# Kernel optimization log

Measured on AMD Instinct MI355X. Metric: run time of the kernel, lower is better.

Reference implementation:

```python
import jax, jax.numpy as jnp
import numpy as np

H, KVH, D, BS, L = 32, 8, 128, 16, 4096
MAX_BLOCKS = L // BS          # 256 blocks per sequence (sink cache capacity)
B = 16
NUM_BLOCKS = B * MAX_BLOCKS   # 4096 total cache blocks
T = MAX_BLOCKS * BS           # 4096 linearized cache slots per sequence
SCALE = 1.0 / np.sqrt(D)


def _rope_cos_sin(pos):
    # neox-style RoPE tables; pos: int array [...]. returns cos/sin [..., D/2]
    inv_freq = 1.0 / (10000.0 ** (jnp.arange(0, D, 2, dtype=jnp.float32) / D))
    ang = pos[..., None].astype(jnp.float32) * inv_freq
    return jnp.cos(ang), jnp.sin(ang)


def _apply_rope(x, cos, sin):
    # x [..., D]; cos/sin broadcastable to x[..., :D//2]
    x1, x2 = jnp.split(x, 2, axis=-1)
    return jnp.concatenate([x1 * cos - x2 * sin, x2 * cos + x1 * sin], axis=-1)


def setup_inputs() -> dict:
    key = jax.random.key(0)
    ks = jax.random.split(key, 6)
    q = jax.random.normal(ks[0], (B, H * D), dtype=jnp.float32)
    k = jax.random.normal(ks[1], (B, KVH * D), dtype=jnp.float32)
    v = jax.random.normal(ks[2], (B, KVH * D), dtype=jnp.float32)
    key_cache = jax.random.normal(ks[3], (NUM_BLOCKS, BS, KVH, D), dtype=jnp.float32)
    value_cache = jax.random.normal(ks[4], (NUM_BLOCKS, BS, KVH, D), dtype=jnp.float32)
    block_tables = jnp.arange(B * MAX_BLOCKS, dtype=jnp.int32).reshape(B, MAX_BLOCKS)
    context_lens = jax.random.randint(ks[5], (B,), 0, 6000, dtype=jnp.int32)
    return {"q": q, "k": k, "v": v, "key_cache": key_cache,
            "value_cache": value_cache, "block_tables": block_tables,
            "context_lens": context_lens}


def reference(q, k, v, key_cache, value_cache, block_tables, context_lens):
    ctx = context_lens.astype(jnp.int32)                         # [B] past tokens
    rem = ctx % BS
    # sink/rolling cap: if past >= model_context_len, effective seq len caps
    seq_len = jnp.where(ctx >= L, L - BS + rem + 1, ctx + 1)     # [B]
    pos_q = seq_len - 1                                          # capped current position

    # gather pre-rope keys/values from paged cache -> [B, T, KVH, D]
    keys = key_cache[block_tables].reshape(B, T, KVH, D)
    vals = value_cache[block_tables].reshape(B, T, KVH, D)

    # re-apply rope to gathered keys at their cache-relative positions 0..T-1
    cos_k, sin_k = _rope_cos_sin(jnp.arange(T))                  # [T, D/2]
    keys = _apply_rope(keys, cos_k[None, :, None, :], sin_k[None, :, None, :])

    # rope current q, k at capped positions
    cos_q, sin_q = _rope_cos_sin(pos_q)                          # [B, D/2]
    qh = _apply_rope(q.reshape(B, H, D), cos_q[:, None, :], sin_q[:, None, :])
    kh = _apply_rope(k.reshape(B, KVH, D), cos_q[:, None, :], sin_q[:, None, :])

    # scatter current token's k/v at its slot (offset rem in last used block == seq_len-1)
    bidx = jnp.arange(B)
    keys = keys.at[bidx, pos_q].set(kh)
    vals = vals.at[bidx, pos_q].set(v.reshape(B, KVH, D))

    # GQA attention over first seq_len cached tokens
    G = H // KVH
    qg = qh.reshape(B, KVH, G, D)
    scores = jnp.einsum('bhgd,bthd->bhgt', qg, keys) * SCALE     # [B, KVH, G, T]
    mask = jnp.arange(T)[None, :] < seq_len[:, None]             # [B, T]
    scores = jnp.where(mask[:, None, None, :], scores, jnp.finfo(scores.dtype).min)
    probs = jax.nn.softmax(scores, axis=-1)
    out = jnp.einsum('bhgt,bthd->bhgd', probs, vals)             # [B, KVH, G, D]
    return out.reshape(B, H * D)
```

## Files before the change

### kernel.cpp

```cpp
#include <hip/hip_runtime.h>
#include <math.h>

#define B_      16
#define H_      32
#define KVH_    8
#define G_      4
#define D_      128
#define BS_     16
#define L_      4096
#define MAXB_   256
#define T_      4096
#define NPART_  16
#define PART_   256
#define SCALE_  0.08838834764831843f

__device__ __forceinline__ int seq_len_of(int ctx) {
  return (ctx >= L_) ? (L_ - BS_ + (ctx & (BS_ - 1)) + 1) : (ctx + 1);
}


#define LOADK(P, tt)                                                        \
  {                                                                         \
    int blk_  = sblk[((tt) - t0) >> 4];                                     \
    int base_ = ((blk_ * BS_ + ((tt) & (BS_ - 1))) * KVH_ + kvh) * D_;      \
    const float4* kc4_ = (const float4*)(kc + base_);                       \
    const float4* vc4_ = (const float4*)(vc + base_);                       \
    P##ka = kc4_[dg];      P##kb = kc4_[16 + dg];                           \
    P##va = vc4_[dg];      P##vb = vc4_[16 + dg];                           \
  }

#define COMPUTE(P, tt)                                                      \
  {                                                                         \
    float kr1[4], kr2[4];                                                   \
    kr1[0] = P##ka.x * cc0.x - P##kb.x * cc0.y;                             \
    kr2[0] = P##kb.x * cc0.x + P##ka.x * cc0.y;                             \
    kr1[1] = P##ka.y * cc0.z - P##kb.y * cc0.w;                             \
    kr2[1] = P##kb.y * cc0.z + P##ka.y * cc0.w;                             \
    kr1[2] = P##ka.z * cc1.x - P##kb.z * cc1.y;                             \
    kr2[2] = P##kb.z * cc1.x + P##ka.z * cc1.y;                             \
    kr1[3] = P##ka.w * cc1.z - P##kb.w * cc1.w;                             \
    kr2[3] = P##kb.w * cc1.z + P##ka.w * cc1.w;                             \
    bool valid_ = ((tt) != posq);                                           \
    float s[G_];                                                            \
    _Pragma("unroll")                                                       \
    for (int g = 0; g < G_; ++g) {                                          \
      s[g] = kr1[0] * q1[g][0] + kr2[0] * q2[g][0]                          \
           + kr1[1] * q1[g][1] + kr2[1] * q2[g][1]                          \
           + kr1[2] * q1[g][2] + kr2[2] * q2[g][2]                          \
           + kr1[3] * q1[g][3] + kr2[3] * q2[g][3];                         \
    }                                                                       \
    _Pragma("unroll")                                                       \
    for (int off = 1; off <= 8; off <<= 1) {                                \
      _Pragma("unroll")                                                     \
      for (int g = 0; g < G_; ++g) s[g] += __shfl_xor(s[g], off);           \
    }                                                                       \
    _Pragma("unroll")                                                       \
    for (int g = 0; g < G_; ++g) {                                          \
      float sv   = valid_ ? s[g] : -1e30f;                                  \
      float mn   = fmaxf(m[g], sv);                                         \
      float corr = __expf(m[g] - mn);                                       \
      float p    = __expf(sv - mn);                                         \
      p = valid_ ? p : 0.0f;                                                \
      m[g] = mn;                                                            \
      l[g] = l[g] * corr + p;                                               \
      acc[g][0] = acc[g][0] * corr + p * P##va.x;                           \
      acc[g][1] = acc[g][1] * corr + p * P##va.y;                           \
      acc[g][2] = acc[g][2] * corr + p * P##va.z;                           \
      acc[g][3] = acc[g][3] * corr + p * P##va.w;                           \
      acc[g][4] = acc[g][4] * corr + p * P##vb.x;                           \
      acc[g][5] = acc[g][5] * corr + p * P##vb.y;                           \
      acc[g][6] = acc[g][6] * corr + p * P##vb.z;                           \
      acc[g][7] = acc[g][7] * corr + p * P##vb.w;                           \
    }                                                                       \
    {                     \
      float nc_;                                                            \
      nc_ = cc0.x * r0.x - cc0.y * r0.y;                                    \
      cc0.y = cc0.y * r0.x + cc0.x * r0.y; cc0.x = nc_;                     \
      nc_ = cc0.z * r0.z - cc0.w * r0.w;                                    \
      cc0.w = cc0.w * r0.z + cc0.z * r0.w; cc0.z = nc_;                     \
      nc_ = cc1.x * r1.x - cc1.y * r1.y;                                    \
      cc1.y = cc1.y * r1.x + cc1.x * r1.y; cc1.x = nc_;                     \
      nc_ = cc1.z * r1.z - cc1.w * r1.w;                                    \
      cc1.w = cc1.w * r1.z + cc1.z * r1.w; cc1.z = nc_;                     \
    }                                                                       \
  }

__global__ __launch_bounds__(256) void attn_partial_kernel(
    const float* __restrict__ q, const float* __restrict__ knew,
    const float* __restrict__ vnew, const float* __restrict__ kc,
    const float* __restrict__ vc, const int* __restrict__ btab,
    const int* __restrict__ ctxl,
    float* __restrict__ opart, float2* __restrict__ ml) {
  int bid  = blockIdx.x;
  int part = bid & (NPART_ - 1);
  int kvh  = (bid >> 4) & (KVH_ - 1);
  int b    = bid >> 7;

  int seq = seq_len_of(ctxl[b]);
  int t0 = part * PART_;
  if (t0 >= seq) return;
  int t1 = min(t0 + PART_, seq);
  int posq = seq - 1;

  int lane = threadIdx.x & 63;
  int wave = threadIdx.x >> 6;
  int tsub = lane >> 4;
  int dg   = lane & 15;

  __shared__ int sblk[PART_ / BS_];
  if (threadIdx.x < PART_ / BS_)
    sblk[threadIdx.x] = btab[b * MAXB_ + (t0 >> 4) + threadIdx.x];
  __syncthreads();

  int tstart = t0 + 4 * wave + tsub;
  float4 cc0, cc1, r0, r1, cq0, cq1;
  {
    float ft = (float)tstart, fq = (float)posq;
    float cs[3][8];
#pragma unroll
    for (int j = 0; j < 4; ++j) {
      double invd = pow(10000.0, -(double)(8 * dg + 2 * j) / 128.0);
      float invf = (float)invd;
      float angs[3] = {ft * invf, 16.0f * invf, fq * invf};
#pragma unroll
      for (int u = 0; u < 3; ++u) {
        double sn, csn;
        sincos((double)angs[u], &sn, &csn);
        cs[u][2 * j]     = (float)csn;
        cs[u][2 * j + 1] = (float)sn;
      }
    }
    cc0 = make_float4(cs[0][0], cs[0][1], cs[0][2], cs[0][3]);
    cc1 = make_float4(cs[0][4], cs[0][5], cs[0][6], cs[0][7]);
    r0  = make_float4(cs[1][0], cs[1][1], cs[1][2], cs[1][3]);
    r1  = make_float4(cs[1][4], cs[1][5], cs[1][6], cs[1][7]);
    cq0 = make_float4(cs[2][0], cs[2][1], cs[2][2], cs[2][3]);
    cq1 = make_float4(cs[2][4], cs[2][5], cs[2][6], cs[2][7]);
  }

  float q1[G_][4], q2[G_][4];
#pragma unroll
  for (int g = 0; g < G_; ++g) {
    const float* qp = q + b * (H_ * D_) + (kvh * G_ + g) * D_;
    float4 a  = *(const float4*)(qp + 4 * dg);
    float4 bq = *(const float4*)(qp + 64 + 4 * dg);
    q1[g][0] = (a.x * cq0.x - bq.x * cq0.y) * SCALE_;
    q2[g][0] = (bq.x * cq0.x + a.x * cq0.y) * SCALE_;
    q1[g][1] = (a.y * cq0.z - bq.y * cq0.w) * SCALE_;
    q2[g][1] = (bq.y * cq0.z + a.y * cq0.w) * SCALE_;
    q1[g][2] = (a.z * cq1.x - bq.z * cq1.y) * SCALE_;
    q2[g][2] = (bq.z * cq1.x + a.z * cq1.y) * SCALE_;
    q1[g][3] = (a.w * cq1.z - bq.w * cq1.w) * SCALE_;
    q2[g][3] = (bq.w * cq1.z + a.w * cq1.w) * SCALE_;
  }

  float m[G_], l[G_], acc[G_][8];
#pragma unroll
  for (int g = 0; g < G_; ++g) {
    m[g] = -1e30f; l[g] = 0.f;
#pragma unroll
    for (int j = 0; j < 8; ++j) acc[g][j] = 0.f;
  }

  {
    float4 Aka, Akb, Ava, Avb;
    float4 Bka, Bkb, Bva, Bvb;
    int t = tstart;
    if (t < t1) {
      LOADK(A, t);
      while (1) {
        int t2 = t + 16;
        if (t2 < t1) LOADK(B, t2);
        COMPUTE(A, t);
        t = t2;
        if (t >= t1) break;
        t2 = t + 16;
        if (t2 < t1) LOADK(A, t2);
        COMPUTE(B, t);
        t = t2;
        if (t >= t1) break;
      }
    }
  }

  if (threadIdx.x < 16 && posq >= t0 && posq < t1) {
    const float* kp = knew + (b * KVH_ + kvh) * D_;
    float4 xa = *(const float4*)(kp + 4 * dg);
    float4 xb = *(const float4*)(kp + 64 + 4 * dg);
    float kr1[4], kr2[4];
    kr1[0] = xa.x * cq0.x - xb.x * cq0.y;  kr2[0] = xb.x * cq0.x + xa.x * cq0.y;
    kr1[1] = xa.y * cq0.z - xb.y * cq0.w;  kr2[1] = xb.y * cq0.z + xa.y * cq0.w;
    kr1[2] = xa.z * cq1.x - xb.z * cq1.y;  kr2[2] = xb.z * cq1.x + xa.z * cq1.y;
    kr1[3] = xa.w * cq1.z - xb.w * cq1.w;  kr2[3] = xb.w * cq1.z + xa.w * cq1.w;
    const float* vp = vnew + (b * KVH_ + kvh) * D_;
    float4 va_ = *(const float4*)(vp + 4 * dg);
    float4 vb_ = *(const float4*)(vp + 64 + 4 * dg);
    float s[G_];
#pragma unroll
    for (int g = 0; g < G_; ++g) {
      s[g] = kr1[0] * q1[g][0] + kr2[0] * q2[g][0]
           + kr1[1] * q1[g][1] + kr2[1] * q2[g][1]
           + kr1[2] * q1[g][2] + kr2[2] * q2[g][2]
           + kr1[3] * q1[g][3] + kr2[3] * q2[g][3];
    }
#pragma unroll
    for (int off = 1; off <= 8; off <<= 1) {
#pragma unroll
      for (int g = 0; g < G_; ++g) s[g] += __shfl_xor(s[g], off);
    }
#pragma unroll
    for (int g = 0; g < G_; ++g) {
      float sv   = s[g];
      float mn   = fmaxf(m[g], sv);
      float corr = __expf(m[g] - mn);
      float p    = __expf(sv - mn);
      m[g] = mn;
      l[g] = l[g] * corr + p;
      acc[g][0] = acc[g][0] * corr + p * va_.x;
      acc[g][1] = acc[g][1] * corr + p * va_.y;
      acc[g][2] = acc[g][2] * corr + p * va_.z;
      acc[g][3] = acc[g][3] * corr + p * va_.w;
      acc[g][4] = acc[g][4] * corr + p * vb_.x;
      acc[g][5] = acc[g][5] * corr + p * vb_.y;
      acc[g][6] = acc[g][6] * corr + p * vb_.z;
      acc[g][7] = acc[g][7] * corr + p * vb_.w;
    }
  }

  auto merge_off = [&](int off) {
#pragma unroll
    for (int g = 0; g < G_; ++g) {
      float mo = __shfl_xor(m[g], off);
      float lo = __shfl_xor(l[g], off);
      float M  = fmaxf(m[g], mo);
      float fa = __expf(m[g] - M);
      float fb = __expf(mo - M);
      l[g] = l[g] * fa + lo * fb;
      m[g] = M;
#pragma unroll
      for (int j = 0; j < 8; ++j) {
        float ao = __shfl_xor(acc[g][j], off);
        acc[g][j] = acc[g][j] * fa + ao * fb;
      }
    }
  };
  merge_off(16);
  merge_off(32);

  __shared__ float  lds_acc[4][G_][D_];
  __shared__ float2 lds_ml[4][G_];
  if (lane < 16) {
#pragma unroll
    for (int g = 0; g < G_; ++g) {
#pragma unroll
      for (int j = 0; j < 8; ++j) {
        int dim = (j < 4) ? (4 * dg + j) : (64 + 4 * dg + (j - 4));
        lds_acc[wave][g][dim] = acc[g][j];
      }
      if (lane == 0) lds_ml[wave][g] = make_float2(m[g], l[g]);
    }
  }
  __syncthreads();
  if (wave == 0) {
    int w = tsub;
#pragma unroll
    for (int g = 0; g < G_; ++g) {
      float2 t2 = lds_ml[w][g];
      m[g] = t2.x; l[g] = t2.y;
#pragma unroll
      for (int j = 0; j < 8; ++j) {
        int dim = (j < 4) ? (4 * dg + j) : (64 + 4 * dg + (j - 4));
        acc[g][j] = lds_acc[w][g][dim];
      }
    }
    merge_off(16);
    merge_off(32);
    if (lane < 16) {
#pragma unroll
      for (int g = 0; g < G_; ++g) {
        float* op = opart + (size_t)((bid)*G_ + g) * D_;
#pragma unroll
        for (int j = 0; j < 8; ++j) {
          int dim = (j < 4) ? (4 * dg + j) : (64 + 4 * dg + (j - 4));
          op[dim] = acc[g][j];
        }
        if (lane == 0) ml[bid * G_ + g] = make_float2(m[g], l[g]);
      }
    }
  }
}

__global__ void attn_reduce_kernel(const float* __restrict__ opart,
                                   const float2* __restrict__ ml,
                                   const int* __restrict__ ctxl,
                                   float* __restrict__ out) {
  int bh = blockIdx.x;
  int b = bh >> 5, h = bh & 31;
  int kvh = h >> 2, g = h & 3;
  int d = threadIdx.x;
  int seq = seq_len_of(ctxl[b]);
  int nlive = (seq + PART_ - 1) / PART_;
  int base = (b * KVH_ + kvh) * NPART_;

  float M = -1e30f;
  for (int p = 0; p < nlive; ++p) M = fmaxf(M, ml[(base + p) * G_ + g].x);
  float L = 0.f, O = 0.f;
  for (int p = 0; p < nlive; ++p) {
    float2 mlv = ml[(base + p) * G_ + g];
    float f = __expf(mlv.x - M);
    L += mlv.y * f;
    O += opart[(size_t)((base + p) * G_ + g) * D_ + d] * f;
  }
  out[b * (H_ * D_) + h * D_ + d] = O / L;
}

extern "C" void kernel_launch(void* const* d_in, const int* in_sizes, int n_in,
                              void* d_out, int out_size, void* d_ws, size_t ws_size,
                              hipStream_t stream) {
  const float* q    = (const float*)d_in[0];
  const float* k    = (const float*)d_in[1];
  const float* v    = (const float*)d_in[2];
  const float* kc   = (const float*)d_in[3];
  const float* vc   = (const float*)d_in[4];
  const int*   btab = (const int*)d_in[5];
  const int*   ctxl = (const int*)d_in[6];
  float* out = (float*)d_out;

  float*  opart = (float*)d_ws;
  float2* ml    = (float2*)(opart + (size_t)B_ * KVH_ * NPART_ * G_ * D_);

  attn_partial_kernel<<<B_ * KVH_ * NPART_, 256, 0, stream>>>(
      q, k, v, kc, vc, btab, ctxl, opart, ml);
  attn_reduce_kernel<<<B_ * H_, D_, 0, stream>>>(opart, ml, ctxl, out);
}
```

Baseline: 119.2 us.

## Split sequence into more partitions, remap block order, branch online-softmax rescale

Doubles the number of sequence partitions (each partition now covers 128 tokens) so the grid has more work groups to fill the GPU. It also remaps blockIdx so that consecutive groups of 8 blocks cover different KV heads of the same partition, which changes the cache and scheduling locality. The online-softmax update is split into a branch so the common no-new-max case skips the rescale exp and multiplies. In exchange the reduce kernel must merge more partials, more partial data is written to the workspace, and the branch can diverge within a wave.

```diff
diff --git a/kernel.cpp b/kernel.cpp
--- a/kernel.cpp
+++ b/kernel.cpp
@@ -10,8 +10,9 @@
 #define L_      4096
 #define MAXB_   256
 #define T_      4096
-#define NPART_  16
-#define PART_   256
+#define NPART_  32
+#define PART_   128
+#define GRID_   (B_ * KVH_ * NPART_)
 #define SCALE_  0.08838834764831843f
 
 __device__ __forceinline__ int seq_len_of(int ctx) {
@@ -56,21 +57,32 @@
     }                                                                       \
     _Pragma("unroll")                                                       \
     for (int g = 0; g < G_; ++g) {                                          \
-      float sv   = valid_ ? s[g] : -1e30f;                                  \
-      float mn   = fmaxf(m[g], sv);                                         \
-      float corr = __expf(m[g] - mn);                                       \
-      float p    = __expf(sv - mn);                                         \
-      p = valid_ ? p : 0.0f;                                                \
-      m[g] = mn;                                                            \
-      l[g] = l[g] * corr + p;                                               \
-      acc[g][0] = acc[g][0] * corr + p * P##va.x;                           \
-      acc[g][1] = acc[g][1] * corr + p * P##va.y;                           \
-      acc[g][2] = acc[g][2] * corr + p * P##va.z;                           \
-      acc[g][3] = acc[g][3] * corr + p * P##va.w;                           \
-      acc[g][4] = acc[g][4] * corr + p * P##vb.x;                           \
-      acc[g][5] = acc[g][5] * corr + p * P##vb.y;                           \
-      acc[g][6] = acc[g][6] * corr + p * P##vb.z;                           \
-      acc[g][7] = acc[g][7] * corr + p * P##vb.w;                           \
+      float sv = valid_ ? s[g] : -1e30f;                                    \
+      if (sv > m[g]) {                \
+        float corr = __expf(m[g] - sv);                                     \
+        l[g] = l[g] * corr + 1.0f;                                          \
+        acc[g][0] = acc[g][0] * corr + P##va.x;                             \
+        acc[g][1] = acc[g][1] * corr + P##va.y;                             \
+        acc[g][2] = acc[g][2] * corr + P##va.z;                             \
+        acc[g][3] = acc[g][3] * corr + P##va.w;                             \
+        acc[g][4] = acc[g][4] * corr + P##vb.x;                             \
+        acc[g][5] = acc[g][5] * corr + P##vb.y;                             \
+        acc[g][6] = acc[g][6] * corr + P##vb.z;                             \
+        acc[g][7] = acc[g][7] * corr + P##vb.w;                             \
+        m[g] = sv;                                                          \
+      } else {                                                              \
+        float p = __expf(sv - m[g]);                                        \
+        p = valid_ ? p : 0.0f;                                              \
+        l[g] += p;                                                          \
+        acc[g][0] += p * P##va.x;                                           \
+        acc[g][1] += p * P##va.y;                                           \
+        acc[g][2] += p * P##va.z;                                           \
+        acc[g][3] += p * P##va.w;                                           \
+        acc[g][4] += p * P##vb.x;                                           \
+        acc[g][5] += p * P##vb.y;                                           \
+        acc[g][6] += p * P##vb.z;                                           \
+        acc[g][7] += p * P##vb.w;                                           \
+      }                                                                     \
     }                                                                       \
     {                     \
       float nc_;                                                            \
@@ -91,10 +103,14 @@
     const float* __restrict__ vc, const int* __restrict__ btab,
     const int* __restrict__ ctxl,
     float* __restrict__ opart, float2* __restrict__ ml) {
-  int bid  = blockIdx.x;
-  int part = bid & (NPART_ - 1);
-  int kvh  = (bid >> 4) & (KVH_ - 1);
-  int b    = bid >> 7;
+  int p    = blockIdx.x;
+  int x    = p & 7;
+  int i    = p >> 3;
+  int grp  = x + (i & ~7);
+  int kvh  = i & 7;
+  int part = grp & (NPART_ - 1);
+  int b    = grp >> 5;
+  int bid  = (b * KVH_ + kvh) * NPART_ + part;
 
   int seq = seq_len_of(ctxl[b]);
   int t0 = part * PART_;
@@ -278,7 +294,7 @@
     if (lane < 16) {
 #pragma unroll
       for (int g = 0; g < G_; ++g) {
-        float* op = opart + (size_t)((bid)*G_ + g) * D_;
+        float* op = opart + (size_t)(bid * G_ + g) * D_;
 #pragma unroll
         for (int j = 0; j < 8; ++j) {
           int dim = (j < 4) ? (4 * dg + j) : (64 + 4 * dg + (j - 4));
@@ -329,7 +345,7 @@
   float*  opart = (float*)d_ws;
   float2* ml    = (float2*)(opart + (size_t)B_ * KVH_ * NPART_ * G_ * D_);
 
-  attn_partial_kernel<<<B_ * KVH_ * NPART_, 256, 0, stream>>>(
+  attn_partial_kernel<<<GRID_, 256, 0, stream>>>(
       q, k, v, kc, vc, btab, ctxl, opart, ml);
   attn_reduce_kernel<<<B_ * H_, D_, 0, stream>>>(opart, ml, ctxl, out);
 }
```

Result: slower. 150.9 us (+26.5%).
